# Kernel tuning notes

Hardware: AMD Instinct MI355X
Metric: run time of the kernel (lower is better)

## Reference

```python
import jax, jax.numpy as jnp
import numpy as np

NEG = -1000000000.0
EPS = 1e-05

def setup_inputs() -> dict:
    key = jax.random.key(0)
    k1, k2, k3, k4, k5 = jax.random.split(key, 5)
    B, L, E, Q = 64, 2048, 512, 256
    encoded_vecs = jax.random.normal(k1, (B, L, E), dtype=jnp.float32)
    query = jax.random.normal(k2, (B, Q), dtype=jnp.float32)
    length = jax.random.randint(k3, (B,), 1, L + 1, dtype=jnp.int32)
    # Xavier-normal-ish params
    W1 = jax.random.normal(k4, (E + Q, E), dtype=jnp.float32) * jnp.sqrt(2.0 / (E + Q + E))
    b1 = jnp.zeros((E,), dtype=jnp.float32)
    v = jax.random.normal(k5, (E,), dtype=jnp.float32) * jnp.sqrt(2.0 / (E + 1))
    return {"encoded_vecs": encoded_vecs, "query": query, "length": length,
            "W1": W1, "b1": b1, "v": v}

def reference(encoded_vecs, query, length, W1, b1, v):
    B, L, E = encoded_vecs.shape
    # broadcast 2D query over the length dim (repeat in torch code)
    q = jnp.broadcast_to(query[:, None, :], (B, L, query.shape[-1]))
    h = jnp.concatenate([encoded_vecs, q], axis=2)            # [B, L, E+Q]
    u = jnp.tanh(jnp.einsum('blc,ce->ble', h, W1) + b1)       # [B, L, E]
    logits = jnp.einsum('ble,e->bl', u, v)                    # [B, L]
    # masked softmax (faithful to masked_softmax in source)
    mask = (jnp.arange(L)[None, :] < length[:, None])         # [B, L] bool
    masked_logits = jnp.where(mask, logits, NEG)
    max_logits = jnp.max(masked_logits, axis=1, keepdims=True)
    exps = jnp.exp(masked_logits - max_logits) * mask.astype(logits.dtype)
    attention = exps / (jnp.sum(exps, axis=1, keepdims=True) + EPS)  # [B, L]
    context = jnp.einsum('bl,ble->be', attention, encoded_vecs)      # [B, E]
    return (context, attention)
```

## Files before the change

kernel.cpp:

```cpp
#include <hip/hip_runtime.h>

typedef __attribute__((ext_vector_type(4))) float float4v;
typedef __attribute__((ext_vector_type(2))) float float2v;
typedef __attribute__((ext_vector_type(8))) short short8;
typedef __attribute__((ext_vector_type(4))) float f32x4;
typedef __attribute__((ext_vector_type(4))) int int4v;

#define NEGV (-1000000000.0f)


__device__ __forceinline__ unsigned short f2bf(float f) {
    unsigned int u = __float_as_uint(f);
    u += 0x7fffu + ((u >> 16) & 1u);
    return (unsigned short)(u >> 16);
}

__device__ __forceinline__ void gload_lds16(const void* g, void* l) {
    __builtin_amdgcn_global_load_lds(
        (__attribute__((address_space(1))) unsigned int*)(unsigned long long)(g),
        (__attribute__((address_space(3))) unsigned int*)(unsigned int)(unsigned long long)(l),
        16, 0, 0);
}

__global__ void prep_wt_kernel(const float* __restrict__ W1, unsigned short* __restrict__ Wt) {
    int idx = blockIdx.x * 256 + threadIdx.x;
    int c = idx >> 9;
    int e = idx & 511;
    Wt[e * 512 + c] = f2bf(W1[idx]);
}

__global__ void prep_qc_kernel(const float* __restrict__ query, const float* __restrict__ W1,
                               const float* __restrict__ b1, float* __restrict__ qc) {
    int b = blockIdx.x;
    int e = threadIdx.x;
    float acc0 = b1[e];
    float acc1 = b1[e + 256];
    const float* w = W1 + 512 * 512;
    for (int q = 0; q < 256; ++q) {
        float qv = query[b * 256 + q];
        acc0 += qv * w[q * 512 + e];
        acc1 += qv * w[q * 512 + e + 256];
    }
    qc[b * 512 + e] = acc0;
    qc[b * 512 + e + 256] = acc1;
}

__global__ __launch_bounds__(256)
void gemm_logits_kernel(const float* __restrict__ A,
                        const unsigned short* __restrict__ Wt,
                        const float* __restrict__ qc,
                        const float* __restrict__ v,
                        const int* __restrict__ length,
                        float* __restrict__ logits)
{
    int bid = blockIdx.x;
    int orig = (bid & 7) * 512 + (bid >> 3);
    int bm = orig >> 2;
    int bn = orig & 3;
    int b = bm >> 4;
    int l0 = (bm & 15) * 128;
    if (l0 >= length[b]) return;

    __shared__ float As[128 * 32];
    __shared__ unsigned short Bs[128 * 32];

    int tid = threadIdx.x;
    int lane = tid & 63;
    int w = tid >> 6;
    int wm = w >> 1, wn = w & 1;
    long row0 = (long)bm * 128;
    int col0 = bn * 128;

    const char* gA[4];
    const char* gB[2];
    #pragma unroll
    for (int i = 0; i < 4; ++i) {
        int off = (w * 4 + i) * 1024 + lane * 16;
        int r = off >> 7;
        int kbs = off & 127;
        int kbg = kbs ^ ((r & 7) << 4);
        gA[i] = (const char*)A + (row0 + r) * 2048 + kbg;
    }
    #pragma unroll
    for (int i = 0; i < 2; ++i) {
        int off = (w * 2 + i) * 1024 + lane * 16;
        int n = off >> 6;
        int kb = off & 63;
        gB[i] = (const char*)Wt + (long)(col0 + n) * 1024 + kb;
    }
    char* lA0 = (char*)As + (w * 4) * 1024;
    char* lB0 = (char*)Bs + (w * 2) * 1024;

    int aoff[4][2], boff[4];
    int kb0 = 32 * (lane >> 4);
    #pragma unroll
    for (int mi = 0; mi < 4; ++mi) {
        int ar = wm * 64 + (lane & 15) + mi * 16;
        int swz = (ar & 7) << 4;
        aoff[mi][0] = ar * 128 + (kb0 ^ swz);
        aoff[mi][1] = ar * 128 + ((kb0 + 16) ^ swz);
    }
    int kbB = 16 * (lane >> 4);
    #pragma unroll
    for (int ni = 0; ni < 4; ++ni) {
        int br = wn * 64 + (lane & 15) + ni * 16;
        boff[ni] = br * 64 + kbB;
    }

    f32x4 acc[4][4] = {};

    for (int ks = 0; ks < 16; ++ks) {
        gload_lds16(gA[0], lA0);
        gload_lds16(gA[1], lA0 + 1024);
        gload_lds16(gA[2], lA0 + 2048);
        gload_lds16(gA[3], lA0 + 3072);
        gload_lds16(gB[0], lB0);
        gload_lds16(gB[1], lB0 + 1024);
        #pragma unroll
        for (int i = 0; i < 4; ++i) gA[i] += 128;
        #pragma unroll
        for (int i = 0; i < 2; ++i) gB[i] += 64;
        __syncthreads();

        short8 af[4], bf[4];
        #pragma unroll
        for (int mi = 0; mi < 4; ++mi) {
            float4v x = *(const float4v*)((const char*)As + aoff[mi][0]);
            float4v y = *(const float4v*)((const char*)As + aoff[mi][1]);
            union { int4v i; short8 s; } u;
            asm("v_cvt_pk_bf16_f32 %0, %1, %2" : "=v"(u.i.x) : "v"(x[0]), "v"(x[1]));
            asm("v_cvt_pk_bf16_f32 %0, %1, %2" : "=v"(u.i.y) : "v"(x[2]), "v"(x[3]));
            asm("v_cvt_pk_bf16_f32 %0, %1, %2" : "=v"(u.i.z) : "v"(y[0]), "v"(y[1]));
            asm("v_cvt_pk_bf16_f32 %0, %1, %2" : "=v"(u.i.w) : "v"(y[2]), "v"(y[3]));
            af[mi] = u.s;
        }
        #pragma unroll
        for (int ni = 0; ni < 4; ++ni)
            bf[ni] = *(const short8*)((const char*)Bs + boff[ni]);

        #pragma unroll
        for (int mi = 0; mi < 4; ++mi)
            #pragma unroll
            for (int ni = 0; ni < 4; ++ni)
                acc[mi][ni] = __builtin_amdgcn_mfma_f32_16x16x32_bf16(af[mi], bf[ni], acc[mi][ni], 0, 0, 0);
        __syncthreads();
    }

    const float* qcb = qc + b * 512;
    float vcol[4], qcol[4];
    #pragma unroll
    for (int ni = 0; ni < 4; ++ni) {
        int c = col0 + wn * 64 + ni * 16 + (lane & 15);
        vcol[ni] = v[c];
        qcol[ni] = qcb[c];
    }
    int rbase = wm * 64 + 4 * (lane >> 4);
    #pragma unroll
    for (int mi = 0; mi < 4; ++mi) {
        #pragma unroll
        for (int j = 0; j < 4; ++j) {
            float s = 0.f;
            #pragma unroll
            for (int ni = 0; ni < 4; ++ni) {
                float x = acc[mi][ni][j] + qcol[ni];
                float e2 = __expf(2.0f * x);
                float t = 1.0f - 2.0f * __builtin_amdgcn_rcpf(e2 + 1.0f);
                s += t * vcol[ni];
            }
            s += __shfl_xor(s, 1);
            s += __shfl_xor(s, 2);
            s += __shfl_xor(s, 4);
            s += __shfl_xor(s, 8);
            if ((lane & 15) == 0) {
                atomicAdd(&logits[row0 + rbase + mi * 16 + j], s);
            }
        }
    }
}

__global__ void softmax_kernel(const float* __restrict__ logits, const int* __restrict__ length,
                               float* __restrict__ att) {
    int b = blockIdx.x;
    int len = length[b];
    int tid = threadIdx.x;
    int lane = tid & 63, wv = tid >> 6;
    const float* lg = logits + b * 2048;
    float* ab = att + b * 2048;

    float vals[8];
    float mymax = -3.402823466e38f;
    #pragma unroll
    for (int i = 0; i < 8; ++i) {
        int l = tid + i * 256;
        float x = (l < len) ? lg[l] : NEGV;
        vals[i] = x;
        mymax = fmaxf(mymax, x);
    }
    #pragma unroll
    for (int m = 32; m; m >>= 1) mymax = fmaxf(mymax, __shfl_xor(mymax, m));
    __shared__ float sm[4];
    if (lane == 0) sm[wv] = mymax;
    __syncthreads();
    float bmax = fmaxf(fmaxf(sm[0], sm[1]), fmaxf(sm[2], sm[3]));

    float mysum = 0.f;
    #pragma unroll
    for (int i = 0; i < 8; ++i) {
        int l = tid + i * 256;
        float e = (l < len) ? __expf(vals[i] - bmax) : 0.f;
        vals[i] = e;
        mysum += e;
    }
    #pragma unroll
    for (int m = 32; m; m >>= 1) mysum += __shfl_xor(mysum, m);
    __shared__ float ss[4];
    if (lane == 0) ss[wv] = mysum;
    __syncthreads();
    float tot = ss[0] + ss[1] + ss[2] + ss[3];
    float inv = 1.0f / (tot + 1e-5f);
    #pragma unroll
    for (int i = 0; i < 8; ++i) {
        int l = tid + i * 256;
        ab[l] = vals[i] * inv;
    }
}

__global__ void ctx_kernel(const float* __restrict__ att, const float* __restrict__ enc,
                           const int* __restrict__ length, float* __restrict__ ctx) {
    int b = blockIdx.x;
    int lc = blockIdx.y;
    int len = length[b];
    int l0 = lc * 128;
    if (l0 >= len) return;
    int lim = len - l0;
    if (lim > 128) lim = 128;

    int t = threadIdx.x;
    const float* ab = att + b * 2048 + l0;
    const float* eb = enc + ((long)(b * 2048 + l0)) * 512 + t * 2;
    float c0 = 0.f, c1 = 0.f;
    #pragma unroll 4
    for (int l = 0; l < lim; ++l) {
        float a = ab[l];
        float2v e = *(const float2v*)(eb);
        eb += 512;
        c0 += a * e.x;
        c1 += a * e.y;
    }
    atomicAdd(&ctx[b * 512 + 2 * t], c0);
    atomicAdd(&ctx[b * 512 + 2 * t + 1], c1);
}

extern "C" void kernel_launch(void* const* d_in, const int* in_sizes, int n_in,
                              void* d_out, int out_size, void* d_ws, size_t ws_size,
                              hipStream_t stream) {
    const float* enc    = (const float*)d_in[0];
    const float* query  = (const float*)d_in[1];
    const int*   length = (const int*)d_in[2];
    const float* W1     = (const float*)d_in[3];
    const float* b1     = (const float*)d_in[4];
    const float* v      = (const float*)d_in[5];

    float* out = (float*)d_out;
    float* ctx = out;
    float* att = out + 64 * 512;

    char* ws = (char*)d_ws;
    float* logits      = (float*)ws;
    float* qc          = (float*)(ws + 64 * 2048 * 4);
    unsigned short* Wt = (unsigned short*)(ws + 64 * 2048 * 4 + 64 * 512 * 4);

    hipMemsetAsync(logits, 0, 64 * 2048 * 4, stream);
    hipMemsetAsync(ctx, 0, 64 * 512 * 4, stream);

    prep_wt_kernel<<<(512 * 512) / 256, 256, 0, stream>>>(W1, Wt);
    prep_qc_kernel<<<64, 256, 0, stream>>>(query, W1, b1, qc);

    gemm_logits_kernel<<<4096, 256, 0, stream>>>(enc, Wt, qc, v, length, logits);

    softmax_kernel<<<64, 256, 0, stream>>>(logits, length, att);

    dim3 g3(64, 16);
    ctx_kernel<<<g3, 256, 0, stream>>>(att, enc, length, ctx);
}
```

Measured before the change: 151.4 us.

## Double-buffer GEMM LDS, replace logit atomics with partial slices, tile weight transpose

The GEMM main loop now uses two LDS buffers, so the next K-tile's global-to-LDS load is issued before computing on the current one, which halves the barriers per tile. Logit partial sums are written to eight per-column-slice buffers instead of being atomically added. The softmax kernel sums those slices and also zeroes ctx, which removes both memsets. The weight transpose now goes through a shared-memory tile so its global accesses coalesce. The cost is double the LDS per block, which may lower occupancy, plus eight reads per logit in softmax.

```diff
diff --git a/kernel.cpp b/kernel.cpp
--- a/kernel.cpp
+++ b/kernel.cpp
@@ -8,6 +8,7 @@
 
 #define NEGV (-1000000000.0f)
 
+#define MTOT (64 * 2048)
 
 __device__ __forceinline__ unsigned short f2bf(float f) {
     unsigned int u = __float_as_uint(f);
@@ -22,11 +23,20 @@
         16, 0, 0);
 }
 
-__global__ void prep_wt_kernel(const float* __restrict__ W1, unsigned short* __restrict__ Wt) {
-    int idx = blockIdx.x * 256 + threadIdx.x;
-    int c = idx >> 9;
-    int e = idx & 511;
-    Wt[e * 512 + c] = f2bf(W1[idx]);
+__global__ __launch_bounds__(256)
+void prep_wt_kernel(const float* __restrict__ W1, unsigned short* __restrict__ Wt) {
+    __shared__ float t[32][33];
+    int bx = blockIdx.x & 15;
+    int by = blockIdx.x >> 4;
+    int tx = threadIdx.x & 31;
+    int ty = threadIdx.x >> 5;
+    #pragma unroll
+    for (int i = 0; i < 4; ++i)
+        t[ty + 8 * i][tx] = W1[(bx * 32 + ty + 8 * i) * 512 + by * 32 + tx];
+    __syncthreads();
+    #pragma unroll
+    for (int i = 0; i < 4; ++i)
+        Wt[(by * 32 + ty + 8 * i) * 512 + bx * 32 + tx] = f2bf(t[tx][ty + 8 * i]);
 }
 
 __global__ void prep_qc_kernel(const float* __restrict__ query, const float* __restrict__ W1,
@@ -51,7 +61,7 @@
                         const float* __restrict__ qc,
                         const float* __restrict__ v,
                         const int* __restrict__ length,
-                        float* __restrict__ logits)
+                        float* __restrict__ part)
 {
     int bid = blockIdx.x;
     int orig = (bid & 7) * 512 + (bid >> 3);
@@ -61,8 +71,8 @@
     int l0 = (bm & 15) * 128;
     if (l0 >= length[b]) return;
 
-    __shared__ float As[128 * 32];
-    __shared__ unsigned short Bs[128 * 32];
+    __shared__ float As[2][128 * 32];
+    __shared__ unsigned short Bs[2][128 * 32];
 
     int tid = threadIdx.x;
     int lane = tid & 63;
@@ -77,19 +87,18 @@
     for (int i = 0; i < 4; ++i) {
         int off = (w * 4 + i) * 1024 + lane * 16;
         int r = off >> 7;
-        int kbs = off & 127;
-        int kbg = kbs ^ ((r & 7) << 4);
+        int kbg = (off & 127) ^ ((r & 7) << 4);
         gA[i] = (const char*)A + (row0 + r) * 2048 + kbg;
     }
     #pragma unroll
     for (int i = 0; i < 2; ++i) {
         int off = (w * 2 + i) * 1024 + lane * 16;
-        int n = off >> 6;
-        int kb = off & 63;
-        gB[i] = (const char*)Wt + (long)(col0 + n) * 1024 + kb;
-    }
-    char* lA0 = (char*)As + (w * 4) * 1024;
-    char* lB0 = (char*)Bs + (w * 2) * 1024;
+        gB[i] = (const char*)Wt + (long)(col0 + (off >> 6)) * 1024 + (off & 63);
+    }
+    char* lA0 = (char*)&As[0][0] + w * 4096;
+    char* lA1 = (char*)&As[1][0] + w * 4096;
+    char* lB0 = (char*)&Bs[0][0] + w * 2048;
+    char* lB1 = (char*)&Bs[1][0] + w * 2048;
 
     int aoff[4][2], boff[4];
     int kb0 = 32 * (lane >> 4);
@@ -102,31 +111,25 @@
     }
     int kbB = 16 * (lane >> 4);
     #pragma unroll
-    for (int ni = 0; ni < 4; ++ni) {
-        int br = wn * 64 + (lane & 15) + ni * 16;
-        boff[ni] = br * 64 + kbB;
-    }
+    for (int ni = 0; ni < 4; ++ni)
+        boff[ni] = (wn * 64 + (lane & 15) + ni * 16) * 64 + kbB;
 
     f32x4 acc[4][4] = {};
 
-    for (int ks = 0; ks < 16; ++ks) {
-        gload_lds16(gA[0], lA0);
-        gload_lds16(gA[1], lA0 + 1024);
-        gload_lds16(gA[2], lA0 + 2048);
-        gload_lds16(gA[3], lA0 + 3072);
-        gload_lds16(gB[0], lB0);
-        gload_lds16(gB[1], lB0 + 1024);
-        #pragma unroll
-        for (int i = 0; i < 4; ++i) gA[i] += 128;
-        #pragma unroll
-        for (int i = 0; i < 2; ++i) gB[i] += 64;
-        __syncthreads();
-
+    auto STAGE = [&](int t, char* la, char* lb) {
+        gload_lds16(gA[0] + t * 128, la);
+        gload_lds16(gA[1] + t * 128, la + 1024);
+        gload_lds16(gA[2] + t * 128, la + 2048);
+        gload_lds16(gA[3] + t * 128, la + 3072);
+        gload_lds16(gB[0] + t * 64, lb);
+        gload_lds16(gB[1] + t * 64, lb + 1024);
+    };
+    auto COMPUTE = [&](const float* as, const unsigned short* bs) {
         short8 af[4], bf[4];
         #pragma unroll
         for (int mi = 0; mi < 4; ++mi) {
-            float4v x = *(const float4v*)((const char*)As + aoff[mi][0]);
-            float4v y = *(const float4v*)((const char*)As + aoff[mi][1]);
+            float4v x = *(const float4v*)((const char*)as + aoff[mi][0]);
+            float4v y = *(const float4v*)((const char*)as + aoff[mi][1]);
             union { int4v i; short8 s; } u;
             asm("v_cvt_pk_bf16_f32 %0, %1, %2" : "=v"(u.i.x) : "v"(x[0]), "v"(x[1]));
             asm("v_cvt_pk_bf16_f32 %0, %1, %2" : "=v"(u.i.y) : "v"(x[2]), "v"(x[3]));
@@ -136,13 +139,23 @@
         }
         #pragma unroll
         for (int ni = 0; ni < 4; ++ni)
-            bf[ni] = *(const short8*)((const char*)Bs + boff[ni]);
-
+            bf[ni] = *(const short8*)((const char*)bs + boff[ni]);
         #pragma unroll
         for (int mi = 0; mi < 4; ++mi)
             #pragma unroll
             for (int ni = 0; ni < 4; ++ni)
                 acc[mi][ni] = __builtin_amdgcn_mfma_f32_16x16x32_bf16(af[mi], bf[ni], acc[mi][ni], 0, 0, 0);
+    };
+
+    STAGE(0, lA0, lB0);
+    __syncthreads();
+    #pragma unroll 1
+    for (int ks = 0; ks < 16; ks += 2) {
+        STAGE(ks + 1, lA1, lB1);
+        COMPUTE(&As[0][0], &Bs[0][0]);
+        __syncthreads();
+        if (ks + 2 < 16) STAGE(ks + 2, lA0, lB0);
+        COMPUTE(&As[1][0], &Bs[1][0]);
         __syncthreads();
     }
 
@@ -154,6 +167,7 @@
         vcol[ni] = v[c];
         qcol[ni] = qcb[c];
     }
+    float* pslice = part + (bn * 2 + wn) * MTOT + row0;
     int rbase = wm * 64 + 4 * (lane >> 4);
     #pragma unroll
     for (int mi = 0; mi < 4; ++mi) {
@@ -171,28 +185,36 @@
             s += __shfl_xor(s, 2);
             s += __shfl_xor(s, 4);
             s += __shfl_xor(s, 8);
-            if ((lane & 15) == 0) {
-                atomicAdd(&logits[row0 + rbase + mi * 16 + j], s);
-            }
+            if ((lane & 15) == 0)
+                pslice[rbase + mi * 16 + j] = s;
         }
     }
 }
 
-__global__ void softmax_kernel(const float* __restrict__ logits, const int* __restrict__ length,
-                               float* __restrict__ att) {
+__global__ void softmax_kernel(const float* __restrict__ part, const int* __restrict__ length,
+                               float* __restrict__ att, float* __restrict__ ctx) {
     int b = blockIdx.x;
     int len = length[b];
     int tid = threadIdx.x;
     int lane = tid & 63, wv = tid >> 6;
-    const float* lg = logits + b * 2048;
+    const float* p0 = part + b * 2048;
     float* ab = att + b * 2048;
+
+    ctx[b * 512 + tid] = 0.f;
+    ctx[b * 512 + 256 + tid] = 0.f;
 
     float vals[8];
     float mymax = -3.402823466e38f;
     #pragma unroll
     for (int i = 0; i < 8; ++i) {
         int l = tid + i * 256;
-        float x = (l < len) ? lg[l] : NEGV;
+        float x = NEGV;
+        if (l < len) {
+            x = 0.f;
+            #pragma unroll
+            for (int s = 0; s < 8; ++s)
+                x += p0[s * MTOT + l];
+        }
         vals[i] = x;
         mymax = fmaxf(mymax, x);
     }
@@ -266,19 +288,16 @@
     float* att = out + 64 * 512;
 
     char* ws = (char*)d_ws;
-    float* logits      = (float*)ws;
-    float* qc          = (float*)(ws + 64 * 2048 * 4);
-    unsigned short* Wt = (unsigned short*)(ws + 64 * 2048 * 4 + 64 * 512 * 4);
-
-    hipMemsetAsync(logits, 0, 64 * 2048 * 4, stream);
-    hipMemsetAsync(ctx, 0, 64 * 512 * 4, stream);
-
-    prep_wt_kernel<<<(512 * 512) / 256, 256, 0, stream>>>(W1, Wt);
+    float* part        = (float*)ws;
+    float* qc          = (float*)(ws + 8 * MTOT * 4);
+    unsigned short* Wt = (unsigned short*)(ws + 8 * MTOT * 4 + 64 * 512 * 4);
+
+    prep_wt_kernel<<<256, 256, 0, stream>>>(W1, Wt);
     prep_qc_kernel<<<64, 256, 0, stream>>>(query, W1, b1, qc);
 
-    gemm_logits_kernel<<<4096, 256, 0, stream>>>(enc, Wt, qc, v, length, logits);
-
-    softmax_kernel<<<64, 256, 0, stream>>>(logits, length, att);
+    gemm_logits_kernel<<<4096, 256, 0, stream>>>(enc, Wt, qc, v, length, part);
+
+    softmax_kernel<<<64, 256, 0, stream>>>(part, length, att, ctx);
 
     dim3 g3(64, 16);
     ctx_kernel<<<g3, 256, 0, stream>>>(att, enc, length, ctx);
```

New measurement: 146.1 us. -3.5%, faster.
